# Performance work log

Measured on AMD Instinct MI355X. Metric: run time of the kernel, lower is better.

Reference implementation:

```python
import jax, jax.numpy as jnp
import numpy as np

S, B, IN_DIM, HID, NT, TAPELEN = 256, 64, 128, 128, 2, 128
DIM = HID // NT          # per-tape cell width
LH = HID // 2            # LSTM hidden per direction


def _uniform(k, shape, fan):
    bound = 1.0 / np.sqrt(fan)
    return jax.random.uniform(k, shape, jnp.float32, -bound, bound)


def setup_inputs() -> dict:
    key = jax.random.key(0)
    ks = jax.random.split(key, 17)
    return {
        "inputs": jax.random.normal(ks[0], (S, B, IN_DIM), jnp.float32),
        "tapelen": TAPELEN,
        # bidirectional LSTM (torch gate order i,f,g,o)
        "W_ih_f": _uniform(ks[1], (4 * LH, IN_DIM), LH),
        "W_hh_f": _uniform(ks[2], (4 * LH, LH), LH),
        "b_ih_f": _uniform(ks[3], (4 * LH,), LH),
        "b_hh_f": _uniform(ks[4], (4 * LH,), LH),
        "W_ih_r": _uniform(ks[5], (4 * LH, IN_DIM), LH),
        "W_hh_r": _uniform(ks[6], (4 * LH, LH), LH),
        "b_ih_r": _uniform(ks[7], (4 * LH,), LH),
        "b_hh_r": _uniform(ks[8], (4 * LH,), LH),
        "W_act": _uniform(ks[9], (8 * NT, HID), HID),
        "b_act": _uniform(ks[10], (8 * NT,), HID),
        "W_val": _uniform(ks[11], (DIM * NT, IN_DIM), IN_DIM),
        "b_val": _uniform(ks[12], (DIM * NT,), IN_DIM),
        "W_out": _uniform(ks[13], (HID, HID), HID),
        "b_out": _uniform(ks[14], (HID,), HID),
    }


def _lstm_dir(x, Wih, Whh, bih, bhh, reverse):
    Hh = Whh.shape[1]
    bsz = x.shape[1]
    bias = bih + bhh

    def step(carry, xt):
        h, c = carry
        g = xt @ Wih.T + h @ Whh.T + bias
        i, f, gg, o = jnp.split(g, 4, axis=-1)
        c = jax.nn.sigmoid(f) * c + jax.nn.sigmoid(i) * jnp.tanh(gg)
        h = jax.nn.sigmoid(o) * jnp.tanh(c)
        return (h, c), h

    init = (jnp.zeros((bsz, Hh), x.dtype), jnp.zeros((bsz, Hh), x.dtype))
    _, hs = jax.lax.scan(step, init, x, reverse=reverse)
    return hs


def _nam_forward(inputs, tapelen, W_ih_f, W_hh_f, b_ih_f, b_hh_f,
                 W_ih_r, W_hh_r, b_ih_r, b_hh_r,
                 W_act, b_act, W_val, b_val, W_out, b_out):
    seqlen, bsz, _ = inputs.shape
    n_tapes = W_act.shape[0] // 8
    dim = W_val.shape[0] // n_tapes

    values = (inputs @ W_val.T + b_val).reshape(seqlen, bsz, n_tapes, dim)

    h_fwd = _lstm_dir(inputs, W_ih_f, W_hh_f, b_ih_f, b_hh_f, reverse=False)
    h_rev = _lstm_dir(inputs, W_ih_r, W_hh_r, b_ih_r, b_hh_r, reverse=True)
    hidden_control = jnp.concatenate([h_fwd, h_rev], axis=-1)  # [S,B,HID]

    actions = (hidden_control @ W_act.T + b_act).reshape(seqlen, bsz, n_tapes, 8)
    dir_r = jax.nn.softmax(actions[..., :3], axis=-1)
    dir_w = jax.nn.softmax(actions[..., 3:6], axis=-1)
    rwprobs = jax.nn.sigmoid(actions[..., 6:])

    tape0 = jnp.zeros((tapelen, bsz, n_tapes, dim), inputs.dtype)
    pos0 = jnp.zeros((tapelen, bsz, n_tapes), inputs.dtype).at[0].set(1.0)

    def step(carry, xs):
        tape, rpos, wpos = carry
        val, rdir, wdir, rw = xs  # [B,T,C], [B,T,3], [B,T,3], [B,T,2]
        oldval = jnp.einsum('lntc,lnt->ntc', tape, wpos)
        newmem = jnp.einsum('lnt,ntc->lntc', wpos, val - oldval)
        tape = tape + newmem * rw[None, :, :, 1:2]
        # NOTE: faithful to original — write-position shift uses rolls of rpos
        next_w = jnp.roll(rpos, 1, axis=0)
        prev_w = jnp.roll(rpos, -1, axis=0)
        wpos = (prev_w * wdir[None, :, :, 0] + wpos * wdir[None, :, :, 1]
                + next_w * wdir[None, :, :, 2])
        read_out = jnp.einsum('lntc,lnt->ntc', tape, rpos * rw[None, :, :, 0])
        next_r = jnp.roll(rpos, 1, axis=0)
        prev_r = jnp.roll(rpos, -1, axis=0)
        rpos = (prev_r * rdir[None, :, :, 0] + rpos * rdir[None, :, :, 1]
                + next_r * rdir[None, :, :, 2])
        return (tape, rpos, wpos), read_out

    (tape, rpos, wpos), read_outs = jax.lax.scan(
        step, (tape0, pos0, pos0), (values, dir_r, dir_w, rwprobs))

    outputs = read_outs.reshape(seqlen, bsz, -1) @ W_out.T + b_out
    return outputs, tape, rpos, wpos


def reference(inputs, tapelen, W_ih_f, W_hh_f, b_ih_f, b_hh_f,
              W_ih_r, W_hh_r, b_ih_r, b_hh_r,
              W_act, b_act, W_val, b_val, W_out, b_out):
    return _nam_forward(inputs, tapelen, W_ih_f, W_hh_f, b_ih_f, b_hh_f,
                        W_ih_r, W_hh_r, b_ih_r, b_hh_r,
                        W_act, b_act, W_val, b_val, W_out, b_out)
```

## Files before the change

### kernel.cpp

```cpp
#include <hip/hip_runtime.h>


typedef unsigned short u16;
typedef __attribute__((ext_vector_type(8))) __bf16 bf16x8;
typedef __attribute__((ext_vector_type(4))) float f32x4;

__device__ __forceinline__ u16 f2bf(float x) {
  unsigned u = __builtin_bit_cast(unsigned, x);
  u += 0x7fffu + ((u >> 16) & 1u);
  return (u16)(u >> 16);
}
__device__ __forceinline__ float sigm_f(float x) { return 1.f / (1.f + __expf(-x)); }
__device__ __forceinline__ float tanh_f(float x) { return 1.f - 2.f / (__expf(2.f * x) + 1.f); }

struct ConvArgs {
  const float* src[8];
  u16* dst[8];
  int off[9];
};

__global__ __launch_bounds__(256) void k_convert(ConvArgs a) {
  int i = blockIdx.x * 256 + threadIdx.x;
  if (i < 524288) {
    float4 vv = ((const float4*)a.src[0])[i];
    uint2 o;
    o.x = (unsigned)f2bf(vv.x) | ((unsigned)f2bf(vv.y) << 16);
    o.y = (unsigned)f2bf(vv.z) | ((unsigned)f2bf(vv.w) << 16);
    ((uint2*)a.dst[0])[i] = o;
  } else if (i < 657408) {
    int ii = i - 524288 + 2097152;
    int s = 1;
#pragma unroll
    for (int k = 2; k < 8; ++k) s += (ii >= a.off[k]);
    int j = ii - a.off[s];
    a.dst[s][j] = f2bf(a.src[s][j]);
  }
}

__device__ __forceinline__ void gemm_tile(const u16* A, const u16* W,
                                          const float* b1, float* C,
                                          int mt, int nt, int N, int lane) {
  const int rc = lane & 15;
  const int kq = lane >> 4;
  f32x4 acc = {0.f, 0.f, 0.f, 0.f};
#pragma unroll
  for (int kc = 0; kc < 4; ++kc) {
    bf16x8 av = *(const bf16x8*)(A + (size_t)(mt * 16 + rc) * 128 + kc * 32 + kq * 8);
    bf16x8 wv = *(const bf16x8*)(W + (size_t)(nt * 16 + rc) * 128 + kc * 32 + kq * 8);
    acc = __builtin_amdgcn_mfma_f32_16x16x32_bf16(av, wv, acc, 0, 0, 0);
  }
  const int n = nt * 16 + rc;
  float bias = b1[n];
  const int m0 = mt * 16 + kq * 4;
#pragma unroll
  for (int j = 0; j < 4; ++j) C[(size_t)(m0 + j) * N + n] = acc[j] + bias;
}

__device__ __forceinline__ void gemm_tile_xp(const u16* A, const u16* W,
                                             const float* b1, const float* b2,
                                             float* X, int mt, int nt, int lane) {
  const int rc = lane & 15;
  const int kq = lane >> 4;
  f32x4 acc = {0.f, 0.f, 0.f, 0.f};
#pragma unroll
  for (int kc = 0; kc < 4; ++kc) {
    bf16x8 av = *(const bf16x8*)(A + (size_t)(mt * 16 + rc) * 128 + kc * 32 + kq * 8);
    bf16x8 wv = *(const bf16x8*)(W + (size_t)(nt * 16 + rc) * 128 + kc * 32 + kq * 8);
    acc = __builtin_amdgcn_mfma_f32_16x16x32_bf16(av, wv, acc, 0, 0, 0);
  }
  const int n = nt * 16 + rc;
  const float bias = b1[n] + b2[n];
  const int m0 = mt * 16 + kq * 4;
  const int s = m0 >> 6, brow0 = m0 & 63;
  const int cb = brow0 >> 4, kq2 = (brow0 & 15) >> 2;
  const int gt = n >> 6, v2 = (n >> 4) & 3, cl2 = n & 15;
  unsigned off = (((unsigned)(s * 4 + cb) * 4 + kq2) * 64 + v2 * 16 + cl2) * 16 + gt * 4;
  f32x4 o;
#pragma unroll
  for (int j = 0; j < 4; ++j) o[j] = acc[j] + bias;
  *(f32x4*)(X + off) = o;
}

__global__ __launch_bounds__(256) void k_gemm_in(
    const u16* __restrict__ Abf, const u16* __restrict__ Wf,
    const u16* __restrict__ Wr, const u16* __restrict__ Wv,
    const float* bihf, const float* bhhf, const float* bihr, const float* bhhr,
    const float* bval, float* xf, float* xr, float* val) {
  int lane = threadIdx.x & 63;
  int wid = blockIdx.x * 4 + (threadIdx.x >> 6);
  if (wid < 16384) {
    gemm_tile_xp(Abf, Wf, bihf, bhhf, xf, wid >> 4, wid & 15, lane);
  } else if (wid < 32768) {
    int w2 = wid - 16384;
    gemm_tile_xp(Abf, Wr, bihr, bhhr, xr, w2 >> 4, w2 & 15, lane);
  } else {
    int w2 = wid - 32768;
    gemm_tile(Abf, Wv, bval, val, w2 >> 3, w2 & 7, 128, lane);
  }
}

__global__ __launch_bounds__(256) void k_gemm_act(const u16* __restrict__ A,
                                                  const u16* __restrict__ W,
                                                  const float* b1, float* C) {
  int lane = threadIdx.x & 63;
  int wid = blockIdx.x * 4 + (threadIdx.x >> 6);
  gemm_tile(A, W, b1, C, wid, 0, 16, lane);
}

__global__ __launch_bounds__(256) void k_gemm_out(const u16* __restrict__ A,
                                                  const u16* __restrict__ W,
                                                  const float* b1, float* C) {
  int lane = threadIdx.x & 63;
  int wid = blockIdx.x * 4 + (threadIdx.x >> 6);
  gemm_tile(A, W, b1, C, wid >> 3, wid & 7, 128, lane);
}

__global__ __launch_bounds__(256, 1) void k_lstm(
    const u16* __restrict__ Whhf, const u16* __restrict__ Whhr,
    const float* __restrict__ xpf, const float* __restrict__ xpr,
    u16* __restrict__ hidden_bf ) {
  const int tid = threadIdx.x;
  const int lane = tid & 63;
  const int v = __builtin_amdgcn_readfirstlane(tid >> 6);
  const int dir = blockIdx.x & 1;
  const int cb = blockIdx.x >> 1;
  const int b_base = cb * 16;
  const u16* Whh = dir ? Whhr : Whhf;
  const float* xp = dir ? xpr : xpf;

  __shared__ u16 h_lds[2][1024];
  for (int i = tid; i < 1024; i += 256) h_lds[0][i] = 0;

  const int cl = lane & 15;
  const int kq = lane >> 4;
  const int nbase = v * 16 + cl;

  bf16x8 wf[4][2];
#pragma unroll
  for (int gt = 0; gt < 4; ++gt)
#pragma unroll
    for (int kc = 0; kc < 2; ++kc)
      wf[gt][kc] = *(const bf16x8*)(Whh + (size_t)(gt * 64 + nbase) * 64 + kc * 32 + kq * 8);

  float c4[4] = {0.f, 0.f, 0.f, 0.f};

  const unsigned tconst = (unsigned)kq * 1024u + (unsigned)nbase * 16u;
  const int s0i = dir ? 255 : 0, s1i = dir ? 254 : 1;
  unsigned x0off = (unsigned)(s0i * 4 + cb) * 4096u + tconst;
  unsigned x1off = (unsigned)(s1i * 4 + cb) * 4096u + tconst;
  const unsigned xstride = dir ? (unsigned)(-32768) : 32768u;

  const unsigned dsrc = ((unsigned)tid * 8u) ^ ((((unsigned)tid >> 4) & 7u) << 4);
  unsigned hoff = (unsigned)(dir ? 255 : 0) * 16384u +
                  (unsigned)(b_base + (tid >> 4)) * 256u + (unsigned)dir * 128u +
                  ((unsigned)tid & 15u) * 8u;
  const unsigned hstride = dir ? (unsigned)(-16384) : 16384u;

  unsigned aw[4];
#pragma unroll
  for (int j = 0; j < 4; ++j) {
    unsigned r = (unsigned)(kq * 4 + j);
    aw[j] = (r * 128u + (unsigned)nbase * 2u) ^ ((r & 7u) << 4);
  }
  unsigned ar[2];
#pragma unroll
  for (int kc = 0; kc < 2; ++kc)
    ar[kc] = ((unsigned)(cl * 128 + kc * 64 + kq * 16)) ^ (((unsigned)cl & 7u) << 4);

  f32x4 x0[4], x1[4];
#define LOADX(X, OFF)                                                          \
  {                                                                            \
    const f32x4* p_ = (const f32x4*)(xp + OFF);                                \
    X[0] = p_[0]; X[1] = p_[1]; X[2] = p_[2]; X[3] = p_[3];                    \
  }
  LOADX(x0, x0off);
  LOADX(x1, x1off);
  x0off += xstride; x1off += xstride;

#define LSTM_STEP(XB, XOFF, IT, PAR)                                           \
  {                                                                            \
    const int it_ = (IT);                                                      \
    __syncthreads();                                                           \
    if (it_ > 0) {                           \
      uint2 hv2 = *(const uint2*)((const char*)h_lds + ((PAR) << 11) + dsrc);  \
      *(uint2*)((char*)hidden_bf + hoff) = hv2;                                \
      hoff += hstride;                                                         \
    }                                                                          \
    bf16x8 af[2];                                                              \
    _Pragma("unroll") for (int kc = 0; kc < 2; ++kc)                           \
      af[kc] = *(const bf16x8*)((const char*)h_lds + ((PAR) << 11) + ar[kc]);  \
    f32x4 acc[4];                                                              \
    _Pragma("unroll") for (int gt = 0; gt < 4; ++gt)                           \
      acc[gt] = __builtin_amdgcn_mfma_f32_16x16x32_bf16(af[0], wf[gt][0],      \
                                                        XB[gt], 0, 0, 0);      \
    if (it_ + 2 < 256) { LOADX(XB, XOFF); XOFF += xstride; }                   \
    _Pragma("unroll") for (int gt = 0; gt < 4; ++gt)                           \
      acc[gt] = __builtin_amdgcn_mfma_f32_16x16x32_bf16(af[1], wf[gt][1],      \
                                                        acc[gt], 0, 0, 0);     \
    float hh[4];                                                               \
    _Pragma("unroll") for (int j = 0; j < 4; ++j) {                            \
      float gi = sigm_f(acc[0][j]);                                            \
      float gf = sigm_f(acc[1][j]);                                            \
      float gg = tanh_f(acc[2][j]);                                            \
      float go = sigm_f(acc[3][j]);                                            \
      float cc = gf * c4[j] + gi * gg;                                         \
      c4[j] = cc;                                                              \
      hh[j] = go * tanh_f(cc);                                                 \
    }                                                                          \
    unsigned p01, p23;                                                         \
    asm("v_cvt_pk_bf16_f32 %0, %1, %2" : "=v"(p01) : "v"(hh[0]), "v"(hh[1]));  \
    asm("v_cvt_pk_bf16_f32 %0, %1, %2" : "=v"(p23) : "v"(hh[2]), "v"(hh[3]));  \
    char* hw = (char*)h_lds + ((1 - (PAR)) << 11);                             \
    *(u16*)(hw + aw[0]) = (u16)p01;                                            \
    *(u16*)(hw + aw[1]) = (u16)(p01 >> 16);                                    \
    *(u16*)(hw + aw[2]) = (u16)p23;                                            \
    *(u16*)(hw + aw[3]) = (u16)(p23 >> 16);                                    \
  }

  for (int it2 = 0; it2 < 256; it2 += 2) {
    LSTM_STEP(x0, x0off, it2, 0);
    LSTM_STEP(x1, x1off, it2 + 1, 1);
  }
#undef LSTM_STEP
#undef LOADX

  __syncthreads();
  {
    uint2 hv2 = *(const uint2*)((const char*)h_lds + dsrc);
    *(uint2*)((char*)hidden_bf + hoff) = hv2;
  }
}

__global__ __launch_bounds__(64) void k_pos(const float* __restrict__ raw,
                                            u16* __restrict__ wcoef, u16* __restrict__ rcoef,
                                            float* rw1arr, float* out_rpos, float* out_wpos) {
  const int bt = blockIdx.x;
  const int l = threadIdx.x;
  const int b = bt >> 1, tt = bt & 1;
  const float* abase = raw + (size_t)b * 16 + tt * 8;
  float4 d0 = *(const float4*)abase;
  float4 d1 = *(const float4*)(abase + 4);
  float rpe = (l == 0) ? 1.f : 0.f, rpo = 0.f;
  float wpe = rpe, wpo = 0.f;
  unsigned* wcu = (unsigned*)wcoef;
  unsigned* rcu = (unsigned*)rcoef;
  for (int s = 0; s < 256; ++s) {
    float m1 = fmaxf(fmaxf(d0.x, d0.y), d0.z);
    float e0 = __expf(d0.x - m1), e1 = __expf(d0.y - m1), e2 = __expf(d0.z - m1);
    float i1 = 1.f / (e0 + e1 + e2);
    float m2 = fmaxf(fmaxf(d0.w, d1.x), d1.y);
    float f0 = __expf(d0.w - m2), f1 = __expf(d1.x - m2), f2 = __expf(d1.y - m2);
    float i2 = 1.f / (f0 + f1 + f2);
    float rd0 = e0 * i1, rd1 = e1 * i1, rd2 = e2 * i1;
    float wd0 = f0 * i2, wd1 = f1 * i2, wd2 = f2 * i2;
    float rw0 = sigm_f(d1.z), rw1 = sigm_f(d1.w);
    if (s + 1 < 256) {
      const float* an = abase + (size_t)(s + 1) * 1024;
      d0 = *(const float4*)an;
      d1 = *(const float4*)(an + 4);
    }
    size_t ci = ((size_t)s * 128 + bt) * 64 + l;
    wcu[ci] = (unsigned)f2bf(wpe) | ((unsigned)f2bf(wpo) << 16);
    rcu[ci] = (unsigned)f2bf(rpe * rw0) | ((unsigned)f2bf(rpo * rw0) << 16);
    if (l == 0) rw1arr[s * 128 + bt] = rw1;
    float up_odd = __shfl(rpo, (l + 63) & 63);
    float dn_even = __shfl(rpe, (l + 1) & 63);
    float n_e = up_odd, n_o = rpe;
    float p_e = rpo, p_o = dn_even;
    wpe = p_e * wd0 + wpe * wd1 + n_e * wd2;
    wpo = p_o * wd0 + wpo * wd1 + n_o * wd2;
    rpe = p_e * rd0 + rpe * rd1 + n_e * rd2;
    rpo = p_o * rd0 + rpo * rd1 + n_o * rd2;
  }
  out_rpos[((size_t)(2 * l) * 64 + b) * 2 + tt] = rpe;
  out_rpos[((size_t)(2 * l + 1) * 64 + b) * 2 + tt] = rpo;
  out_wpos[((size_t)(2 * l) * 64 + b) * 2 + tt] = wpe;
  out_wpos[((size_t)(2 * l + 1) * 64 + b) * 2 + tt] = wpo;
}

__global__ __launch_bounds__(256, 1) void k_tape(
    const float* __restrict__ values, const u16* __restrict__ wcoef,
    const u16* __restrict__ rcoef, const float* __restrict__ rw1arr,
    u16* __restrict__ readouts, float* __restrict__ out_tape) {
  const int bt = blockIdx.x;
  const int b = bt >> 1, t = bt & 1;
  const int tid = threadIdx.x;
  const int c = tid & 63;
  const int g = __builtin_amdgcn_readfirstlane(tid >> 6);
  __shared__ float lds_po[2][256];
  __shared__ float lds_pr[2][256];
  float tape[32];
#pragma unroll
  for (int j = 0; j < 32; ++j) tape[j] = 0.f;

  const unsigned* wcu = (const unsigned*)wcoef;
  const unsigned* rcu = (const unsigned*)rcoef;
  const size_t cbase = (size_t)bt * 64 + g * 16;
  const size_t vbase = (size_t)b * 128 + t * 64 + c;
  unsigned wA[16], rA[16], wB[16], rB[16];
  float rwA, rwB, vA, vB;
#pragma unroll
  for (int q = 0; q < 16; ++q) { wA[q] = wcu[cbase + q]; rA[q] = rcu[cbase + q]; }
  rwA = rw1arr[bt]; vA = values[vbase];
  {
    size_t nb = cbase + 8192;
#pragma unroll
    for (int q = 0; q < 16; ++q) { wB[q] = wcu[nb + q]; rB[q] = rcu[nb + q]; }
    rwB = rw1arr[128 + bt]; vB = values[8192 + vbase];
  }

#define BCF(u) __builtin_bit_cast(float, (u))
#define TSTEP(CW, CR, CRW, CV, S)                                              \
  {                                                                            \
    const int s_ = (S);                                                        \
    float rwc = CRW, vcl = CV;                                                 \
    float po_[4] = {0.f, 0.f, 0.f, 0.f};                                       \
    _Pragma("unroll") for (int q = 0; q < 16; ++q) {                           \
      unsigned cw = (unsigned)__builtin_amdgcn_readfirstlane(CW[q]);           \
      po_[q & 3] += tape[2 * q] * BCF(cw << 16);                               \
      po_[q & 3] += tape[2 * q + 1] * BCF(cw & 0xffff0000u);                   \
    }                                                                          \
    if (s_ + 2 < 256) {                                                        \
      size_t nb = cbase + (size_t)(s_ + 2) * 8192;                             \
      _Pragma("unroll") for (int q = 0; q < 16; ++q) {                         \
        CW[q] = wcu[nb + q]; CR[q] = rcu[nb + q]; }                            \
      CRW = rw1arr[(s_ + 2) * 128 + bt];                                       \
      CV = values[(size_t)(s_ + 2) * 8192 + vbase];                            \
    }                                                                          \
    lds_po[s_ & 1][(g << 6) + c] = (po_[0] + po_[1]) + (po_[2] + po_[3]);      \
    __syncthreads();                                                           \
    if (g == 1 && s_ > 0) {                                                    \
      const float* pp = lds_pr[(s_ - 1) & 1];                                  \
      float ro = (pp[c] + pp[64 + c]) + (pp[128 + c] + pp[192 + c]);           \
      readouts[((size_t)(s_ - 1) * 64 + b) * 128 + t * 64 + c] = f2bf(ro);     \
    }                                                                          \
    const float* qq = lds_po[s_ & 1];                                          \
    float oldv = (qq[c] + qq[64 + c]) + (qq[128 + c] + qq[192 + c]);           \
    float dsc = rwc * (vcl - oldv);                                            \
    float pr_[4] = {0.f, 0.f, 0.f, 0.f};                                       \
    _Pragma("unroll") for (int q = 0; q < 16; ++q) {                           \
      unsigned cw = (unsigned)__builtin_amdgcn_readfirstlane(CW[q]);           \
      unsigned cr = (unsigned)__builtin_amdgcn_readfirstlane(CR[q]);           \
      tape[2 * q] += BCF(cw << 16) * dsc;                                      \
      pr_[q & 3] += tape[2 * q] * BCF(cr << 16);                               \
      tape[2 * q + 1] += BCF(cw & 0xffff0000u) * dsc;                          \
      pr_[q & 3] += tape[2 * q + 1] * BCF(cr & 0xffff0000u);                   \
    }                                                                          \
    lds_pr[s_ & 1][(g << 6) + c] = (pr_[0] + pr_[1]) + (pr_[2] + pr_[3]);      \
  }

  for (int s = 0; s < 256; s += 2) {
    TSTEP(wA, rA, rwA, vA, s);
    TSTEP(wB, rB, rwB, vB, s + 1);
  }
#undef TSTEP
#undef BCF
  __syncthreads();
  if (g == 1) {
    const float* pp = lds_pr[1];
    float ro = (pp[c] + pp[64 + c]) + (pp[128 + c] + pp[192 + c]);
    readouts[((size_t)255 * 64 + b) * 128 + t * 64 + c] = f2bf(ro);
  }
#pragma unroll
  for (int j = 0; j < 32; ++j) {
    int l = (g << 5) + j;
    out_tape[((size_t)(l * 64 + b) * 2 + t) * 64 + c] = tape[j];
  }
}


__global__ __launch_bounds__(256, 1) void k_tape2(
    const float* __restrict__ values, const u16* __restrict__ wcoef,
    const u16* __restrict__ rcoef, const float* __restrict__ rw1arr,
    u16* __restrict__ readouts, float* __restrict__ out_tape) {
  const int bt = blockIdx.x;
  const int b = bt >> 1, t = bt & 1;
  const int tid = threadIdx.x;
  const int c = tid & 63;
  const int g = __builtin_amdgcn_readfirstlane(tid >> 6);
  __shared__ float lds_po[2][256];
  __shared__ float lds_pr[2][256];
  float tape[32];
#pragma unroll
  for (int j = 0; j < 32; ++j) tape[j] = 0.f;

  const unsigned* wcu = (const unsigned*)wcoef;
  const unsigned* rcu = (const unsigned*)rcoef;
  const size_t cbase = (size_t)bt * 64 + g * 16;
  const size_t vbase = (size_t)b * 128 + t * 64 + c;
  unsigned wA[16], rA[16], wB[16], rB[16];
  float rwA, rwB, vA, vB;
#pragma unroll
  for (int q = 0; q < 16; ++q) { wA[q] = wcu[cbase + q]; rA[q] = rcu[cbase + q]; }
  rwA = rw1arr[bt]; vA = values[vbase];
  {
    size_t nb = cbase + 8192;
#pragma unroll
    for (int q = 0; q < 16; ++q) { wB[q] = wcu[nb + q]; rB[q] = rcu[nb + q]; }
    rwB = rw1arr[128 + bt]; vB = values[8192 + vbase];
  }

#define BCF(u) __builtin_bit_cast(float, (u))
#define TSTEP(CW, CR, CRW, CV, S)                                              \
  {                                                                            \
    const int s_ = (S);                                                        \
    float rwc = CRW, vcl = CV;                                                 \
    float wsc[32], rsc[32];                                                    \
    _Pragma("unroll") for (int q = 0; q < 16; ++q) {                           \
      unsigned cw = (unsigned)__builtin_amdgcn_readfirstlane(CW[q]);           \
      unsigned cr = (unsigned)__builtin_amdgcn_readfirstlane(CR[q]);           \
      wsc[2 * q] = BCF(cw << 16);  wsc[2 * q + 1] = BCF(cw & 0xffff0000u);     \
      rsc[2 * q] = BCF(cr << 16);  rsc[2 * q + 1] = BCF(cr & 0xffff0000u);     \
    }                                                                          \
    float po_[4] = {0.f, 0.f, 0.f, 0.f};                                       \
    _Pragma("unroll") for (int j = 0; j < 32; ++j)                             \
      po_[j & 3] += tape[j] * wsc[j];                                          \
    if (s_ + 2 < 256) {                                                        \
      size_t nb = cbase + (size_t)(s_ + 2) * 8192;                             \
      _Pragma("unroll") for (int q = 0; q < 16; ++q) {                         \
        CW[q] = wcu[nb + q]; CR[q] = rcu[nb + q]; }                            \
      CRW = rw1arr[(s_ + 2) * 128 + bt];                                       \
      CV = values[(size_t)(s_ + 2) * 8192 + vbase];                            \
    }                                                                          \
    lds_po[s_ & 1][(g << 6) + c] = (po_[0] + po_[1]) + (po_[2] + po_[3]);      \
    __syncthreads();                                                           \
    if (g == 1 && s_ > 0) {                                                    \
      const float* pp = lds_pr[(s_ - 1) & 1];                                  \
      float ro = (pp[c] + pp[64 + c]) + (pp[128 + c] + pp[192 + c]);           \
      readouts[((size_t)(s_ - 1) * 64 + b) * 128 + t * 64 + c] = f2bf(ro);     \
    }                                                                          \
    const float* qq = lds_po[s_ & 1];                                          \
    float oldv = (qq[c] + qq[64 + c]) + (qq[128 + c] + qq[192 + c]);           \
    float dsc = rwc * (vcl - oldv);                                            \
    float pr_[4] = {0.f, 0.f, 0.f, 0.f};                                       \
    _Pragma("unroll") for (int j = 0; j < 32; ++j) {                           \
      tape[j] += wsc[j] * dsc;                                                 \
      pr_[j & 3] += tape[j] * rsc[j];                                          \
    }                                                                          \
    lds_pr[s_ & 1][(g << 6) + c] = (pr_[0] + pr_[1]) + (pr_[2] + pr_[3]);      \
  }

  for (int s = 0; s < 256; s += 2) {
    TSTEP(wA, rA, rwA, vA, s);
    TSTEP(wB, rB, rwB, vB, s + 1);
  }
#undef TSTEP
#undef BCF
  __syncthreads();
  if (g == 1) {
    const float* pp = lds_pr[1];
    float ro = (pp[c] + pp[64 + c]) + (pp[128 + c] + pp[192 + c]);
    readouts[((size_t)255 * 64 + b) * 128 + t * 64 + c] = f2bf(ro);
  }
#pragma unroll
  for (int j = 0; j < 32; ++j) {
    int l = (g << 5) + j;
    out_tape[((size_t)(l * 64 + b) * 2 + t) * 64 + c] = tape[j];
  }
}

extern "C" void kernel_launch(void* const* d_in, const int* in_sizes, int n_in,
                              void* d_out, int out_size, void* d_ws, size_t ws_size,
                              hipStream_t stream) {
  const float* inputs = (const float*)d_in[0];
  const float* W_ih_f = (const float*)d_in[2];
  const float* W_hh_f = (const float*)d_in[3];
  const float* b_ih_f = (const float*)d_in[4];
  const float* b_hh_f = (const float*)d_in[5];
  const float* W_ih_r = (const float*)d_in[6];
  const float* W_hh_r = (const float*)d_in[7];
  const float* b_ih_r = (const float*)d_in[8];
  const float* b_hh_r = (const float*)d_in[9];
  const float* W_act  = (const float*)d_in[10];
  const float* b_act  = (const float*)d_in[11];
  const float* W_val  = (const float*)d_in[12];
  const float* b_val  = (const float*)d_in[13];
  const float* W_out  = (const float*)d_in[14];
  const float* b_out  = (const float*)d_in[15];

  char* ws = (char*)d_ws;
  u16* in_bf    = (u16*)(ws + 0);
  u16* wihf_bf  = (u16*)(ws + 4194304);
  u16* whhf_bf  = (u16*)(ws + 4259840);
  u16* wihr_bf  = (u16*)(ws + 4292608);
  u16* whhr_bf  = (u16*)(ws + 4358144);
  u16* wval_bf  = (u16*)(ws + 4390912);
  u16* wout_bf  = (u16*)(ws + 4423680);
  u16* wact_bf  = (u16*)(ws + 4456448);
  float* xf       = (float*)(ws + 4460544);
  float* xr       = (float*)(ws + 21237760);
  float* values   = (float*)(ws + 38014976);
  u16* hidden_bf  = (u16*)(ws + 46403584);
  float* actraw   = (float*)(ws + 50597888);
  u16* wcoef    = (u16*)(ws + 4460544);
  u16* rcoef    = (u16*)(ws + 12849152);
  float* rw1arr = (float*)(ws + 21237760);
  u16* readouts = (u16*)(ws + 21368832);

  float* out_outputs = (float*)d_out;
  float* out_tape = out_outputs + 2097152;
  float* out_rpos = out_outputs + 3145728;
  float* out_wpos = out_outputs + 3162112;

  ConvArgs ca;
  ca.src[0] = inputs; ca.dst[0] = in_bf;
  ca.src[1] = W_ih_f; ca.dst[1] = wihf_bf;
  ca.src[2] = W_hh_f; ca.dst[2] = whhf_bf;
  ca.src[3] = W_ih_r; ca.dst[3] = wihr_bf;
  ca.src[4] = W_hh_r; ca.dst[4] = whhr_bf;
  ca.src[5] = W_val;  ca.dst[5] = wval_bf;
  ca.src[6] = W_out;  ca.dst[6] = wout_bf;
  ca.src[7] = W_act;  ca.dst[7] = wact_bf;
  const int offs[9] = {0, 2097152, 2129920, 2146304, 2179072, 2195456,
                       2211840, 2228224, 2230272};
  for (int i = 0; i < 9; ++i) ca.off[i] = offs[i];

  hipLaunchKernelGGL(k_convert, dim3(2568), dim3(256), 0, stream, ca);
  hipLaunchKernelGGL(k_gemm_in, dim3(10240), dim3(256), 0, stream,
                     in_bf, wihf_bf, wihr_bf, wval_bf,
                     b_ih_f, b_hh_f, b_ih_r, b_hh_r, b_val, xf, xr, values);
  hipLaunchKernelGGL(k_lstm, dim3(8), dim3(256), 0, stream,
                     whhf_bf, whhr_bf, xf, xr, hidden_bf);
  hipLaunchKernelGGL(k_gemm_act, dim3(512), dim3(256), 0, stream,
                     hidden_bf, wact_bf, b_act, actraw);
  hipLaunchKernelGGL(k_pos, dim3(128), dim3(64), 0, stream,
                     actraw, wcoef, rcoef, rw1arr, out_rpos, out_wpos);
  hipLaunchKernelGGL(k_tape2, dim3(128), dim3(256), 0, stream,
                     values, wcoef, rcoef, rw1arr, readouts, out_tape);
  hipLaunchKernelGGL(k_gemm_out, dim3(2048), dim3(256), 0, stream,
                     readouts, wout_bf, b_out, out_outputs);
}
```

Before: 678.1 us.

## Rewrite tape kernel as single-wave per tape with fp32 coefficients

The tape recurrence kernel moves from four waves per tape, which exchanged partial sums through LDS and synchronised twice per step, to one 64-lane wave that holds all 128 tape rows in registers as packed float pairs. The position kernel now writes fp32 coefficient pairs instead of packed bf16, so the tape kernel reads coefficients directly with packed FMA and needs no unpacking. Workspace offsets are reassigned for the larger coefficient buffers, and the old k_tape2 variant is removed. The trade is four times fewer waves doing four times the serial work each, plus twice the coefficient traffic, in exchange for removing the barriers and LDS reductions.

```diff
diff --git a/kernel.cpp b/kernel.cpp
--- a/kernel.cpp
+++ b/kernel.cpp
@@ -4,6 +4,7 @@
 typedef unsigned short u16;
 typedef __attribute__((ext_vector_type(8))) __bf16 bf16x8;
 typedef __attribute__((ext_vector_type(4))) float f32x4;
+typedef __attribute__((ext_vector_type(2))) float f32x2;
 
 __device__ __forceinline__ u16 f2bf(float x) {
   unsigned u = __builtin_bit_cast(unsigned, x);
@@ -181,7 +182,7 @@
   {                                                                            \
     const int it_ = (IT);                                                      \
     __syncthreads();                                                           \
-    if (it_ > 0) {                           \
+    if (it_ > 0) {                                                             \
       uint2 hv2 = *(const uint2*)((const char*)h_lds + ((PAR) << 11) + dsrc);  \
       *(uint2*)((char*)hidden_bf + hoff) = hv2;                                \
       hoff += hstride;                                                         \
@@ -232,8 +233,10 @@
 }
 
 __global__ __launch_bounds__(64) void k_pos(const float* __restrict__ raw,
-                                            u16* __restrict__ wcoef, u16* __restrict__ rcoef,
-                                            float* rw1arr, float* out_rpos, float* out_wpos) {
+                                            f32x2* __restrict__ wcoef,
+                                            f32x2* __restrict__ rcoef,
+                                            float* rw1arr, float* out_rpos,
+                                            float* out_wpos) {
   const int bt = blockIdx.x;
   const int l = threadIdx.x;
   const int b = bt >> 1, tt = bt & 1;
@@ -242,8 +245,6 @@
   float4 d1 = *(const float4*)(abase + 4);
   float rpe = (l == 0) ? 1.f : 0.f, rpo = 0.f;
   float wpe = rpe, wpo = 0.f;
-  unsigned* wcu = (unsigned*)wcoef;
-  unsigned* rcu = (unsigned*)rcoef;
   for (int s = 0; s < 256; ++s) {
     float m1 = fmaxf(fmaxf(d0.x, d0.y), d0.z);
     float e0 = __expf(d0.x - m1), e1 = __expf(d0.y - m1), e2 = __expf(d0.z - m1);
@@ -260,8 +261,10 @@
       d1 = *(const float4*)(an + 4);
     }
     size_t ci = ((size_t)s * 128 + bt) * 64 + l;
-    wcu[ci] = (unsigned)f2bf(wpe) | ((unsigned)f2bf(wpo) << 16);
-    rcu[ci] = (unsigned)f2bf(rpe * rw0) | ((unsigned)f2bf(rpo * rw0) << 16);
+    f32x2 wv; wv[0] = wpe; wv[1] = wpo;
+    f32x2 rv; rv[0] = rpe * rw0; rv[1] = rpo * rw0;
+    wcoef[ci] = wv;
+    rcoef[ci] = rv;
     if (l == 0) rw1arr[s * 128 + bt] = rw1;
     float up_odd = __shfl(rpo, (l + 63) & 63);
     float dn_even = __shfl(rpe, (l + 1) & 63);
@@ -278,184 +281,71 @@
   out_wpos[((size_t)(2 * l + 1) * 64 + b) * 2 + tt] = wpo;
 }
 
-__global__ __launch_bounds__(256, 1) void k_tape(
-    const float* __restrict__ values, const u16* __restrict__ wcoef,
-    const u16* __restrict__ rcoef, const float* __restrict__ rw1arr,
+__global__ __launch_bounds__(64, 1) void k_tape(
+    const float* __restrict__ values, const f32x2* __restrict__ wcoef,
+    const f32x2* __restrict__ rcoef, const float* __restrict__ rw1arr,
     u16* __restrict__ readouts, float* __restrict__ out_tape) {
   const int bt = blockIdx.x;
   const int b = bt >> 1, t = bt & 1;
-  const int tid = threadIdx.x;
-  const int c = tid & 63;
-  const int g = __builtin_amdgcn_readfirstlane(tid >> 6);
-  __shared__ float lds_po[2][256];
-  __shared__ float lds_pr[2][256];
-  float tape[32];
-#pragma unroll
-  for (int j = 0; j < 32; ++j) tape[j] = 0.f;
-
-  const unsigned* wcu = (const unsigned*)wcoef;
-  const unsigned* rcu = (const unsigned*)rcoef;
-  const size_t cbase = (size_t)bt * 64 + g * 16;
+  const int c = threadIdx.x;
+
+  f32x2 tp[64];
+#pragma unroll
+  for (int k = 0; k < 64; ++k) { tp[k][0] = 0.f; tp[k][1] = 0.f; }
+
   const size_t vbase = (size_t)b * 128 + t * 64 + c;
-  unsigned wA[16], rA[16], wB[16], rB[16];
-  float rwA, rwB, vA, vB;
-#pragma unroll
-  for (int q = 0; q < 16; ++q) { wA[q] = wcu[cbase + q]; rA[q] = rcu[cbase + q]; }
-  rwA = rw1arr[bt]; vA = values[vbase];
-  {
-    size_t nb = cbase + 8192;
-#pragma unroll
-    for (int q = 0; q < 16; ++q) { wB[q] = wcu[nb + q]; rB[q] = rcu[nb + q]; }
-    rwB = rw1arr[128 + bt]; vB = values[8192 + vbase];
-  }
-
-#define BCF(u) __builtin_bit_cast(float, (u))
-#define TSTEP(CW, CR, CRW, CV, S)                                              \
-  {                                                                            \
-    const int s_ = (S);                                                        \
-    float rwc = CRW, vcl = CV;                                                 \
-    float po_[4] = {0.f, 0.f, 0.f, 0.f};                                       \
-    _Pragma("unroll") for (int q = 0; q < 16; ++q) {                           \
-      unsigned cw = (unsigned)__builtin_amdgcn_readfirstlane(CW[q]);           \
-      po_[q & 3] += tape[2 * q] * BCF(cw << 16);                               \
-      po_[q & 3] += tape[2 * q + 1] * BCF(cw & 0xffff0000u);                   \
-    }                                                                          \
-    if (s_ + 2 < 256) {                                                        \
-      size_t nb = cbase + (size_t)(s_ + 2) * 8192;                             \
-      _Pragma("unroll") for (int q = 0; q < 16; ++q) {                         \
-        CW[q] = wcu[nb + q]; CR[q] = rcu[nb + q]; }                            \
-      CRW = rw1arr[(s_ + 2) * 128 + bt];                                       \
-      CV = values[(size_t)(s_ + 2) * 8192 + vbase];                            \
-    }                                                                          \
-    lds_po[s_ & 1][(g << 6) + c] = (po_[0] + po_[1]) + (po_[2] + po_[3]);      \
-    __syncthreads();                                                           \
-    if (g == 1 && s_ > 0) {                                                    \
-      const float* pp = lds_pr[(s_ - 1) & 1];                                  \
-      float ro = (pp[c] + pp[64 + c]) + (pp[128 + c] + pp[192 + c]);           \
-      readouts[((size_t)(s_ - 1) * 64 + b) * 128 + t * 64 + c] = f2bf(ro);     \
-    }                                                                          \
-    const float* qq = lds_po[s_ & 1];                                          \
-    float oldv = (qq[c] + qq[64 + c]) + (qq[128 + c] + qq[192 + c]);           \
-    float dsc = rwc * (vcl - oldv);                                            \
-    float pr_[4] = {0.f, 0.f, 0.f, 0.f};                                       \
-    _Pragma("unroll") for (int q = 0; q < 16; ++q) {                           \
-      unsigned cw = (unsigned)__builtin_amdgcn_readfirstlane(CW[q]);           \
-      unsigned cr = (unsigned)__builtin_amdgcn_readfirstlane(CR[q]);           \
-      tape[2 * q] += BCF(cw << 16) * dsc;                                      \
-      pr_[q & 3] += tape[2 * q] * BCF(cr << 16);                               \
-      tape[2 * q + 1] += BCF(cw & 0xffff0000u) * dsc;                          \
-      pr_[q & 3] += tape[2 * q + 1] * BCF(cr & 0xffff0000u);                   \
-    }                                                                          \
-    lds_pr[s_ & 1][(g << 6) + c] = (pr_[0] + pr_[1]) + (pr_[2] + pr_[3]);      \
-  }
-
-  for (int s = 0; s < 256; s += 2) {
-    TSTEP(wA, rA, rwA, vA, s);
-    TSTEP(wB, rB, rwB, vB, s + 1);
-  }
-#undef TSTEP
-#undef BCF
-  __syncthreads();
-  if (g == 1) {
-    const float* pp = lds_pr[1];
-    float ro = (pp[c] + pp[64 + c]) + (pp[128 + c] + pp[192 + c]);
-    readouts[((size_t)255 * 64 + b) * 128 + t * 64 + c] = f2bf(ro);
-  }
-#pragma unroll
-  for (int j = 0; j < 32; ++j) {
-    int l = (g << 5) + j;
-    out_tape[((size_t)(l * 64 + b) * 2 + t) * 64 + c] = tape[j];
-  }
-}
-
-
-__global__ __launch_bounds__(256, 1) void k_tape2(
-    const float* __restrict__ values, const u16* __restrict__ wcoef,
-    const u16* __restrict__ rcoef, const float* __restrict__ rw1arr,
-    u16* __restrict__ readouts, float* __restrict__ out_tape) {
-  const int bt = blockIdx.x;
-  const int b = bt >> 1, t = bt & 1;
-  const int tid = threadIdx.x;
-  const int c = tid & 63;
-  const int g = __builtin_amdgcn_readfirstlane(tid >> 6);
-  __shared__ float lds_po[2][256];
-  __shared__ float lds_pr[2][256];
-  float tape[32];
-#pragma unroll
-  for (int j = 0; j < 32; ++j) tape[j] = 0.f;
-
-  const unsigned* wcu = (const unsigned*)wcoef;
-  const unsigned* rcu = (const unsigned*)rcoef;
-  const size_t cbase = (size_t)bt * 64 + g * 16;
-  const size_t vbase = (size_t)b * 128 + t * 64 + c;
-  unsigned wA[16], rA[16], wB[16], rB[16];
-  float rwA, rwB, vA, vB;
-#pragma unroll
-  for (int q = 0; q < 16; ++q) { wA[q] = wcu[cbase + q]; rA[q] = rcu[cbase + q]; }
-  rwA = rw1arr[bt]; vA = values[vbase];
-  {
-    size_t nb = cbase + 8192;
-#pragma unroll
-    for (int q = 0; q < 16; ++q) { wB[q] = wcu[nb + q]; rB[q] = rcu[nb + q]; }
-    rwB = rw1arr[128 + bt]; vB = values[8192 + vbase];
-  }
-
-#define BCF(u) __builtin_bit_cast(float, (u))
-#define TSTEP(CW, CR, CRW, CV, S)                                              \
-  {                                                                            \
-    const int s_ = (S);                                                        \
-    float rwc = CRW, vcl = CV;                                                 \
-    float wsc[32], rsc[32];                                                    \
-    _Pragma("unroll") for (int q = 0; q < 16; ++q) {                           \
-      unsigned cw = (unsigned)__builtin_amdgcn_readfirstlane(CW[q]);           \
-      unsigned cr = (unsigned)__builtin_amdgcn_readfirstlane(CR[q]);           \
-      wsc[2 * q] = BCF(cw << 16);  wsc[2 * q + 1] = BCF(cw & 0xffff0000u);     \
-      rsc[2 * q] = BCF(cr << 16);  rsc[2 * q + 1] = BCF(cr & 0xffff0000u);     \
-    }                                                                          \
-    float po_[4] = {0.f, 0.f, 0.f, 0.f};                                       \
-    _Pragma("unroll") for (int j = 0; j < 32; ++j)                             \
-      po_[j & 3] += tape[j] * wsc[j];                                          \
-    if (s_ + 2 < 256) {                                                        \
-      size_t nb = cbase + (size_t)(s_ + 2) * 8192;                             \
-      _Pragma("unroll") for (int q = 0; q < 16; ++q) {                         \
-        CW[q] = wcu[nb + q]; CR[q] = rcu[nb + q]; }                            \
-      CRW = rw1arr[(s_ + 2) * 128 + bt];                                       \
-      CV = values[(size_t)(s_ + 2) * 8192 + vbase];                            \
-    }                                                                          \
-    lds_po[s_ & 1][(g << 6) + c] = (po_[0] + po_[1]) + (po_[2] + po_[3]);      \
-    __syncthreads();                                                           \
-    if (g == 1 && s_ > 0) {                                                    \
-      const float* pp = lds_pr[(s_ - 1) & 1];                                  \
-      float ro = (pp[c] + pp[64 + c]) + (pp[128 + c] + pp[192 + c]);           \
-      readouts[((size_t)(s_ - 1) * 64 + b) * 128 + t * 64 + c] = f2bf(ro);     \
-    }                                                                          \
-    const float* qq = lds_po[s_ & 1];                                          \
-    float oldv = (qq[c] + qq[64 + c]) + (qq[128 + c] + qq[192 + c]);           \
-    float dsc = rwc * (vcl - oldv);                                            \
-    float pr_[4] = {0.f, 0.f, 0.f, 0.f};                                       \
-    _Pragma("unroll") for (int j = 0; j < 32; ++j) {                           \
-      tape[j] += wsc[j] * dsc;                                                 \
-      pr_[j & 3] += tape[j] * rsc[j];                                          \
-    }                                                                          \
-    lds_pr[s_ & 1][(g << 6) + c] = (pr_[0] + pr_[1]) + (pr_[2] + pr_[3]);      \
-  }
-
-  for (int s = 0; s < 256; s += 2) {
-    TSTEP(wA, rA, rwA, vA, s);
-    TSTEP(wB, rB, rwB, vB, s + 1);
-  }
-#undef TSTEP
-#undef BCF
-  __syncthreads();
-  if (g == 1) {
-    const float* pp = lds_pr[1];
-    float ro = (pp[c] + pp[64 + c]) + (pp[128 + c] + pp[192 + c]);
-    readouts[((size_t)255 * 64 + b) * 128 + t * 64 + c] = f2bf(ro);
-  }
-#pragma unroll
-  for (int j = 0; j < 32; ++j) {
-    int l = (g << 5) + j;
-    out_tape[((size_t)(l * 64 + b) * 2 + t) * 64 + c] = tape[j];
+  float vA = values[vbase];
+  float rwA = rw1arr[bt];
+
+  for (int s = 0; s < 256; ++s) {
+    const f32x2* __restrict__ wp = wcoef + ((size_t)s * 128 + bt) * 64;
+    const f32x2* __restrict__ rp = rcoef + ((size_t)s * 128 + bt) * 64;
+    const float vcur = vA;
+    const float rwcur = rwA;
+    if (s + 1 < 256) {
+      vA = values[(size_t)(s + 1) * 8192 + vbase];
+      rwA = rw1arr[(s + 1) * 128 + bt];
+    }
+    f32x2 acc[8];
+#pragma unroll
+    for (int i = 0; i < 8; ++i) { acc[i][0] = 0.f; acc[i][1] = 0.f; }
+#pragma unroll
+    for (int k0 = 0; k0 < 64; k0 += 8) {
+      f32x2 wl[8];
+#pragma unroll
+      for (int q = 0; q < 8; ++q) wl[q] = wp[k0 + q];
+#pragma unroll
+      for (int q = 0; q < 8; ++q) acc[q] += tp[k0 + q] * wl[q];
+    }
+    f32x2 s2 = ((acc[0] + acc[1]) + (acc[2] + acc[3])) +
+               ((acc[4] + acc[5]) + (acc[6] + acc[7]));
+    float oldv = s2[0] + s2[1];
+    float dsc = rwcur * (vcur - oldv);
+    f32x2 dsc2; dsc2[0] = dsc; dsc2[1] = dsc;
+    f32x2 pa[8];
+#pragma unroll
+    for (int i = 0; i < 8; ++i) { pa[i][0] = 0.f; pa[i][1] = 0.f; }
+#pragma unroll
+    for (int k0 = 0; k0 < 64; k0 += 8) {
+      f32x2 wl[8], rl[8];
+#pragma unroll
+      for (int q = 0; q < 8; ++q) { wl[q] = wp[k0 + q]; rl[q] = rp[k0 + q]; }
+#pragma unroll
+      for (int q = 0; q < 8; ++q) {
+        tp[k0 + q] += wl[q] * dsc2;
+        pa[q] += tp[k0 + q] * rl[q];
+      }
+    }
+    f32x2 p2 = ((pa[0] + pa[1]) + (pa[2] + pa[3])) +
+               ((pa[4] + pa[5]) + (pa[6] + pa[7]));
+    float pr = p2[0] + p2[1];
+    readouts[((size_t)s * 64 + b) * 128 + t * 64 + c] = f2bf(pr);
+  }
+
+#pragma unroll
+  for (int k = 0; k < 64; ++k) {
+    out_tape[((size_t)(2 * k) * 128 + b * 2 + t) * 64 + c] = tp[k][0];
+    out_tape[((size_t)(2 * k + 1) * 128 + b * 2 + t) * 64 + c] = tp[k][1];
   }
 }
 
@@ -492,10 +382,10 @@
   float* values   = (float*)(ws + 38014976);
   u16* hidden_bf  = (u16*)(ws + 46403584);
   float* actraw   = (float*)(ws + 50597888);
-  u16* wcoef    = (u16*)(ws + 4460544);
-  u16* rcoef    = (u16*)(ws + 12849152);
-  float* rw1arr = (float*)(ws + 21237760);
-  u16* readouts = (u16*)(ws + 21368832);
+  f32x2* wcoef    = (f32x2*)(ws + 4460544);
+  f32x2* rcoef    = (f32x2*)(ws + 21237760);
+  u16* readouts   = (u16*)(ws + 46403584);
+  float* rw1arr   = (float*)(ws + 52695040);
 
   float* out_outputs = (float*)d_out;
   float* out_tape = out_outputs + 2097152;
@@ -525,7 +415,7 @@
                      hidden_bf, wact_bf, b_act, actraw);
   hipLaunchKernelGGL(k_pos, dim3(128), dim3(64), 0, stream,
                      actraw, wcoef, rcoef, rw1arr, out_rpos, out_wpos);
-  hipLaunchKernelGGL(k_tape2, dim3(128), dim3(256), 0, stream,
+  hipLaunchKernelGGL(k_tape, dim3(128), dim3(64), 0, stream,
                      values, wcoef, rcoef, rw1arr, readouts, out_tape);
   hipLaunchKernelGGL(k_gemm_out, dim3(2048), dim3(256), 0, stream,
                      readouts, wout_bf, b_out, out_outputs);
```

New measurement: 1.209 ms. 1.78x slower.
